# Performance work log

Hardware: AMD Instinct MI355X
Metric: run time of the kernel (lower is better)

Reference implementation:

```python
import jax, jax.numpy as jnp
import numpy as np

D_MODEL, N_LEVELS, N_HEADS, N_POINTS = 256, 3, 8, 2
HEAD_DIM = D_MODEL // N_HEADS
SPATIAL_SHAPES = np.array([[100, 100], [50, 50], [25, 25]], dtype=np.int32)
LEN_IN = int((SPATIAL_SHAPES[:, 0] * SPATIAL_SHAPES[:, 1]).sum())  # 13125
BS, NQ = 16, 900


def setup_inputs() -> dict:
    key = jax.random.key(0)
    ks = jax.random.split(key, 12)
    s = 1.0 / np.sqrt(D_MODEL)
    return {
        "query": jax.random.normal(ks[0], (BS, NQ, N_LEVELS, D_MODEL), jnp.float32),
        "reference_points": jax.random.uniform(ks[1], (BS, NQ, N_LEVELS, 2), jnp.float32),
        "input_flatten": jax.random.normal(ks[2], (BS, LEN_IN, D_MODEL), jnp.float32),
        "input_spatial_shapes": jnp.asarray(SPATIAL_SHAPES),
        "W_value": jax.random.normal(ks[3], (D_MODEL, D_MODEL), jnp.float32) * s,
        "b_value": jnp.zeros((D_MODEL,), jnp.float32),
        "W_off": jax.random.normal(ks[4], (D_MODEL, N_HEADS * N_LEVELS * N_POINTS * 2), jnp.float32) * s * 0.1,
        "b_off": jax.random.normal(ks[5], (N_HEADS * N_LEVELS * N_POINTS * 2,), jnp.float32) * 0.5,
        "W_attn": jax.random.normal(ks[6], (D_MODEL, N_HEADS * N_LEVELS * N_POINTS), jnp.float32) * s,
        "b_attn": jnp.zeros((N_HEADS * N_LEVELS * N_POINTS,), jnp.float32),
        "W_out": jax.random.normal(ks[7], (D_MODEL, D_MODEL), jnp.float32) * s,
        "b_out": jnp.zeros((D_MODEL,), jnp.float32),
    }


def _bilinear_sample(v, loc, H, W):
    """v: (bs, nh, H*W, hd); loc in [0,1]: (bs, nh, N, 2). Zero-pad out of range."""
    hd = v.shape[-1]
    x = loc[..., 0] * W - 0.5
    y = loc[..., 1] * H - 0.5
    x0 = jnp.floor(x)
    y0 = jnp.floor(y)
    out = jnp.zeros(x.shape + (hd,), v.dtype)
    for dx in (0, 1):
        for dy in (0, 1):
            xi = x0 + dx
            yi = y0 + dy
            wgt = (1.0 - jnp.abs(x - xi)) * (1.0 - jnp.abs(y - yi))
            valid = (xi >= 0) & (xi <= W - 1) & (yi >= 0) & (yi <= H - 1)
            xi_c = jnp.clip(xi, 0, W - 1).astype(jnp.int32)
            yi_c = jnp.clip(yi, 0, H - 1).astype(jnp.int32)
            idx = yi_c * W + xi_c  # (bs, nh, N)
            idx = jnp.broadcast_to(idx[..., None], idx.shape + (hd,))
            g = jnp.take_along_axis(v, idx, axis=2)  # (bs, nh, N, hd)
            out = out + g * (wgt * valid.astype(wgt.dtype))[..., None]
    return out


def reference(query, reference_points, input_flatten, input_spatial_shapes,
              W_value, b_value, W_off, b_off, W_attn, b_attn, W_out, b_out):
    bs, nq, fl, _ = query.shape
    shapes = np.asarray(input_spatial_shapes)  # static pyramid shapes

    # value projection: (bs, Len, nh, hd)
    value = (input_flatten @ W_value + b_value).reshape(bs, -1, N_HEADS, HEAD_DIM)

    # sampling offsets: (bs, nq, fl, nh, nl, np, 2)
    offsets = (query @ W_off + b_off).reshape(bs, nq, fl, N_HEADS, N_LEVELS, N_POINTS, 2)
    # attention weights softmax over (nl*np): (bs, nq, fl, nh, nl, np)
    attn = (query @ W_attn + b_attn).reshape(bs, nq, fl, N_HEADS, N_LEVELS * N_POINTS)
    attn = jax.nn.softmax(attn, axis=-1).reshape(bs, nq, fl, N_HEADS, N_LEVELS, N_POINTS)

    # normalized sampling locations: ref + offset / (W_l, H_l)
    normalizer = jnp.asarray(shapes[:, ::-1], jnp.float32)  # (nl, 2) = (W, H)
    loc = reference_points[:, :, :, None, None, None, :] + offsets / normalizer[None, None, None, None, :, None, :]

    splits = np.cumsum([h * w for h, w in shapes])[:-1]
    value_list = jnp.split(value, splits, axis=1)

    out = jnp.zeros((bs, N_HEADS, nq, fl, HEAD_DIM), value.dtype)
    for lvl, (H, W) in enumerate(shapes):
        H, W = int(H), int(W)
        v = jnp.transpose(value_list[lvl], (0, 2, 1, 3))  # (bs, nh, H*W, hd)
        loc_l = jnp.transpose(loc[:, :, :, :, lvl], (0, 3, 1, 2, 4, 5))  # (bs, nh, nq, fl, np, 2)
        loc_flat = loc_l.reshape(bs, N_HEADS, nq * fl * N_POINTS, 2)
        sampled = _bilinear_sample(v, loc_flat, H, W).reshape(bs, N_HEADS, nq, fl, N_POINTS, HEAD_DIM)
        w = jnp.transpose(attn[:, :, :, :, lvl], (0, 3, 1, 2, 4))  # (bs, nh, nq, fl, np)
        out = out + jnp.einsum("bhqfpd,bhqfp->bhqfd", sampled, w)

    out = jnp.transpose(out, (0, 2, 3, 1, 4)).reshape(bs, nq, fl, D_MODEL)
    return out @ W_out + b_out
```

## Files before the change

### kernel.cpp

```cpp
#include <hip/hip_runtime.h>
#include <math.h>

#define D_MODEL   256
#define N_HEADS   8
#define HEAD_DIM  32
#define N_LEVELS  3
#define N_POINTS  2
#define BS        16
#define NQ        900
#define LEN_IN    13125
#define M_Q       (BS * NQ * N_LEVELS)
#define M_V       (BS * LEN_IN)
#define NCAT      144
#define NCATP     256

typedef _Float16 f16x8 __attribute__((ext_vector_type(8)));
typedef _Float16 f16x4 __attribute__((ext_vector_type(4)));
typedef float f32x4 __attribute__((ext_vector_type(4)));

__global__ __launch_bounds__(256) void convert_weight_kernel(
    const float* __restrict__ W, _Float16* __restrict__ Wph,
    _Float16* __restrict__ Wpl, int N, int Npad) {
  const int idx = blockIdx.x * 256 + threadIdx.x;
  if (idx >= Npad * 256) return;
  const int n = idx >> 8;
  const int k = idx & 255;
  const float v = (n < N) ? W[(size_t)k * N + n] : 0.0f;
  const _Float16 h = (_Float16)v;
  const int dst = (((n >> 4) * 32) + (k >> 3)) * 128 + (n & 15) * 8 + (k & 7);
  Wph[dst] = h;
  Wpl[dst] = (_Float16)(v - (float)h);
}

__global__ __launch_bounds__(256) void convert_cat_kernel(
    const float* __restrict__ Woff, const float* __restrict__ Wattn,
    const float* __restrict__ boff, const float* __restrict__ battn,
    _Float16* __restrict__ Wph, _Float16* __restrict__ Wpl,
    float* __restrict__ bcat) {
  const int idx = blockIdx.x * 256 + threadIdx.x;
  if (idx >= NCATP * 256) return;
  const int n = idx >> 8;
  const int k = idx & 255;
  float v = 0.0f;
  if (n < 96) v = Woff[(size_t)k * 96 + n];
  else if (n < NCAT) v = Wattn[(size_t)k * 48 + (n - 96)];
  const _Float16 h = (_Float16)v;
  const int dst = (((n >> 4) * 32) + (k >> 3)) * 128 + (n & 15) * 8 + (k & 7);
  Wph[dst] = h;
  Wpl[dst] = (_Float16)(v - (float)h);
  if (idx < NCAT) bcat[idx] = (idx < 96) ? boff[idx] : battn[idx - 96];
}

template <int FC, int TAG>
__global__ __launch_bounds__(256, 4) void gemm4_kernel(
    const float* __restrict__ A, const _Float16* __restrict__ Bph,
    const _Float16* __restrict__ Bpl, const float* __restrict__ bias,
    float* __restrict__ C, int M, int N) {
  constexpr int K = 256;
  __shared__ _Float16 AhL[64 * 128];
  __shared__ _Float16 AlL[64 * 128];

  const int tid = threadIdx.x;
  const int wid = tid >> 6;
  const int lane = tid & 63;
  const int bx = blockIdx.x;
  const int bm = blockIdx.y * 64;
  const int rsel = lane & 15;
  const int q = (lane >> 4) & 3;
  const int swzx = (rsel & 7) << 4;

  char* AhB = (char*)AhL;
  char* AlB = (char*)AlL;

  const _Float16* bph[FC];
  const _Float16* bpl[FC];
#pragma unroll
  for (int fc = 0; fc < FC; ++fc) {
    const int g = bx * 8 + wid * 2 + fc;
    bph[fc] = Bph + (size_t)g * 4096 + lane * 8;
    bpl[fc] = Bpl + (size_t)g * 4096 + lane * 8;
  }

  f32x4 acc[4][FC];
#pragma unroll
  for (int fr = 0; fr < 4; ++fr)
#pragma unroll
    for (int fc = 0; fc < FC; ++fc) acc[fr][fc] = (f32x4)0.0f;

#pragma unroll
  for (int c = 0; c < 2; ++c) {
    if (c == 1) __syncthreads();
#pragma unroll
    for (int it = 0; it < 8; ++it) {
      const int i = it * 1024 + tid * 4;
      const int row = i >> 7;
      const int col = i & 127;
      float4 v = make_float4(0.f, 0.f, 0.f, 0.f);
      if (bm + row < M)
        v = *reinterpret_cast<const float4*>(
            &A[(size_t)(bm + row) * K + c * 128 + col]);
      f16x4 h, l;
      h[0] = (_Float16)v.x; l[0] = (_Float16)(v.x - (float)h[0]);
      h[1] = (_Float16)v.y; l[1] = (_Float16)(v.y - (float)h[1]);
      h[2] = (_Float16)v.z; l[2] = (_Float16)(v.z - (float)h[2]);
      h[3] = (_Float16)v.w; l[3] = (_Float16)(v.w - (float)h[3]);
      const int byt = row * 256 + ((col * 2) ^ ((row & 7) << 4));
      *reinterpret_cast<f16x4*>(AhB + byt) = h;
      *reinterpret_cast<f16x4*>(AlB + byt) = l;
    }
    __syncthreads();

#pragma unroll
    for (int sl = 0; sl < 4; ++sl) {
      const int s = c * 4 + sl;
      f16x8 bh[FC], bl[FC], afh[4], afl[4];
#pragma unroll
      for (int fc = 0; fc < FC; ++fc) {
        bh[fc] = *reinterpret_cast<const f16x8*>(bph[fc] + s * 512);
        bl[fc] = *reinterpret_cast<const f16x8*>(bpl[fc] + s * 512);
      }
#pragma unroll
      for (int fr = 0; fr < 4; ++fr) {
        const int row = fr * 16 + rsel;
        const int byt = row * 256 + ((sl * 64 + q * 16) ^ swzx);
        afh[fr] = *reinterpret_cast<const f16x8*>(AhB + byt);
        afl[fr] = *reinterpret_cast<const f16x8*>(AlB + byt);
      }
      __builtin_amdgcn_s_setprio(1);
#pragma unroll
      for (int fr = 0; fr < 4; ++fr)
#pragma unroll
        for (int fc = 0; fc < FC; ++fc)
          acc[fr][fc] = __builtin_amdgcn_mfma_f32_16x16x32_f16(
              afh[fr], bh[fc], acc[fr][fc], 0, 0, 0);
#pragma unroll
      for (int fr = 0; fr < 4; ++fr)
#pragma unroll
        for (int fc = 0; fc < FC; ++fc)
          acc[fr][fc] = __builtin_amdgcn_mfma_f32_16x16x32_f16(
              afh[fr], bl[fc], acc[fr][fc], 0, 0, 0);
#pragma unroll
      for (int fr = 0; fr < 4; ++fr)
#pragma unroll
        for (int fc = 0; fc < FC; ++fc)
          acc[fr][fc] = __builtin_amdgcn_mfma_f32_16x16x32_f16(
              afl[fr], bh[fc], acc[fr][fc], 0, 0, 0);
      __builtin_amdgcn_s_setprio(0);
    }
  }

  const int colbase = bx * 128 + wid * 32;
  float bs_[FC];
#pragma unroll
  for (int fc = 0; fc < FC; ++fc) {
    const int col = colbase + fc * 16 + rsel;
    bs_[fc] = (col < N) ? bias[col] : 0.0f;
  }
#pragma unroll
  for (int fr = 0; fr < 4; ++fr)
#pragma unroll
    for (int i = 0; i < 4; ++i) {
      const int row = bm + fr * 16 + (lane >> 4) * 4 + i;
      if (row >= M) continue;
#pragma unroll
      for (int fc = 0; fc < FC; ++fc) {
        const int col = colbase + fc * 16 + rsel;
        if (col < N) C[(size_t)row * N + col] = acc[fr][fc][i] + bs_[fc];
      }
    }
}

__global__ __launch_bounds__(256) void sample2_kernel(
    const float* __restrict__ value, const float* __restrict__ refpts,
    const float* __restrict__ offs_attn, float* __restrict__ out_mid) {
  __shared__ int4   s_off[144];
  __shared__ float4 s_w[144];

  const int bq = blockIdx.x;
  const int b = bq / NQ;
  const int tid = threadIdx.x;

  if (tid < 144) {
    const int fl = tid / 48;
    const int rem = tid - fl * 48;
    const int h = rem / 6;
    const int j = rem - h * 6;
    const int l = j >> 1;

    const int LVL_W[3] = {100, 50, 25};
    const int LVL_BASE[3] = {0, 10000, 12500};
    const int W = LVL_W[l];
    const int base = LVL_BASE[l];
    const float fW = (float)W, fH = (float)W;

    const int row = bq * 3 + fl;
    const float* oa = offs_attn + (size_t)row * NCAT;

    float aw[6];
    float mx = -INFINITY;
#pragma unroll
    for (int jj = 0; jj < 6; ++jj) {
      aw[jj] = oa[96 + h * 6 + jj];
      mx = fmaxf(mx, aw[jj]);
    }
    float ssum = 0.f;
#pragma unroll
    for (int jj = 0; jj < 6; ++jj) ssum += expf(aw[jj] - mx);
    const float wa = expf(aw[j] - mx) / ssum;

    const float rx = refpts[(size_t)row * 2 + 0];
    const float ry = refpts[(size_t)row * 2 + 1];
    const float ox = oa[h * 12 + j * 2 + 0];
    const float oy = oa[h * 12 + j * 2 + 1];
    const float x = (rx + ox / fW) * fW - 0.5f;
    const float y = (ry + oy / fH) * fH - 0.5f;
    const float x0 = floorf(x);
    const float y0 = floorf(y);

    int offv[4];
    float wv[4];
#pragma unroll
    for (int dy = 0; dy < 2; ++dy)
#pragma unroll
      for (int dx = 0; dx < 2; ++dx) {
        const float xi = x0 + (float)dx;
        const float yi = y0 + (float)dy;
        const float wgt = (1.0f - fabsf(x - xi)) * (1.0f - fabsf(y - yi));
        const bool valid = (xi >= 0.f) && (xi <= fW - 1.f) &&
                           (yi >= 0.f) && (yi <= fH - 1.f);
        const int xic = (int)fminf(fmaxf(xi, 0.f), fW - 1.f);
        const int yic = (int)fminf(fmaxf(yi, 0.f), fH - 1.f);
        const int pos = base + yic * W + xic;
        offv[dy * 2 + dx] = pos * 1024;
        wv[dy * 2 + dx] = valid ? wgt * wa : 0.0f;
      }
    s_off[tid] = make_int4(offv[0], offv[1], offv[2], offv[3]);
    s_w[tid] = make_float4(wv[0], wv[1], wv[2], wv[3]);
  }
  __syncthreads();

  const int h = tid >> 5;
  const int d = tid & 31;
  const char* vb = (const char*)value +
                   ((size_t)b * LEN_IN * 256 + h * 32 + d) * 4;

#pragma unroll
  for (int fl = 0; fl < 3; ++fl) {
    float acc = 0.f;
#pragma unroll
    for (int j = 0; j < 6; ++j) {
      const int rec = fl * 48 + h * 6 + j;
      const int4 o = s_off[rec];
      const float4 w = s_w[rec];
      acc = fmaf(w.x, *(const float*)(vb + o.x), acc);
      acc = fmaf(w.y, *(const float*)(vb + o.y), acc);
      acc = fmaf(w.z, *(const float*)(vb + o.z), acc);
      acc = fmaf(w.w, *(const float*)(vb + o.w), acc);
    }
    out_mid[((size_t)bq * 3 + fl) * 256 + tid] = acc;
  }
}

extern "C" void kernel_launch(void* const* d_in, const int* in_sizes, int n_in,
                              void* d_out, int out_size, void* d_ws,
                              size_t ws_size, hipStream_t stream) {
  const float* query   = (const float*)d_in[0];
  const float* refpts  = (const float*)d_in[1];
  const float* in_flat = (const float*)d_in[2];
  const float* W_value = (const float*)d_in[4];
  const float* b_value = (const float*)d_in[5];
  const float* W_off   = (const float*)d_in[6];
  const float* b_off   = (const float*)d_in[7];
  const float* W_attn  = (const float*)d_in[8];
  const float* b_attn  = (const float*)d_in[9];
  const float* W_out   = (const float*)d_in[10];
  const float* b_out   = (const float*)d_in[11];
  float* out = (float*)d_out;

  char* ws = (char*)d_ws;
  float* value     = (float*)ws; ws += (size_t)M_V * 256 * sizeof(float);
  float* out_mid   = (float*)ws; ws += (size_t)M_Q * 256 * sizeof(float);
  float* offs_attn = (float*)ws; ws += (size_t)M_Q * NCAT * sizeof(float);
  _Float16* Wvh = (_Float16*)ws; ws += 256 * 256 * sizeof(_Float16);
  _Float16* Wvl = (_Float16*)ws; ws += 256 * 256 * sizeof(_Float16);
  _Float16* Woh = (_Float16*)ws; ws += 256 * 256 * sizeof(_Float16);
  _Float16* Wol = (_Float16*)ws; ws += 256 * 256 * sizeof(_Float16);
  _Float16* Wch = (_Float16*)ws; ws += NCATP * 256 * sizeof(_Float16);
  _Float16* Wcl = (_Float16*)ws; ws += NCATP * 256 * sizeof(_Float16);
  float* bcat   = (float*)ws;    ws += 256 * sizeof(float);

  const dim3 blk(256);

  convert_weight_kernel<<<dim3(256), blk, 0, stream>>>(W_value, Wvh, Wvl, 256, 256);
  convert_weight_kernel<<<dim3(256), blk, 0, stream>>>(W_out,   Woh, Wol, 256, 256);
  convert_cat_kernel<<<dim3(NCATP), blk, 0, stream>>>(W_off, W_attn, b_off, b_attn,
                                                      Wch, Wcl, bcat);

  gemm4_kernel<2, 1><<<dim3(2, (M_V + 63) / 64), blk, 0, stream>>>(
      in_flat, Wvh, Wvl, b_value, value, M_V, 256);

  gemm4_kernel<2, 2><<<dim3(2, (M_Q + 63) / 64), blk, 0, stream>>>(
      query, Wch, Wcl, bcat, offs_attn, M_Q, NCAT);

  sample2_kernel<<<dim3(BS * NQ), blk, 0, stream>>>(value, refpts, offs_attn,
                                                    out_mid);

  gemm4_kernel<2, 3><<<dim3(2, (M_Q + 63) / 64), blk, 0, stream>>>(
      out_mid, Woh, Wol, b_out, out, M_Q, 256);
}
```

Measured before the change: 777.8 us.

## Store value projection and sampled output in fp16 to halve memory traffic

The value projection is now written as fp16 instead of fp32, and the sampling kernel reads fp16 values and writes its intermediate output as fp16. A new GEMM variant takes fp16 A directly, skipping the hi/lo split of A, and keeps only the hi/lo split of the weights. This roughly halves the bytes moved for the large value tensor and the intermediate, cutting both write and gather bandwidth. The cost is precision: activations are rounded to fp16, which may raise error against the fp32 reference.

```diff
diff --git a/kernel.cpp b/kernel.cpp
--- a/kernel.cpp
+++ b/kernel.cpp
@@ -51,11 +51,11 @@
   if (idx < NCAT) bcat[idx] = (idx < 96) ? boff[idx] : battn[idx - 96];
 }
 
-template <int FC, int TAG>
+template <int FC, int TAG, typename OutT>
 __global__ __launch_bounds__(256, 4) void gemm4_kernel(
     const float* __restrict__ A, const _Float16* __restrict__ Bph,
     const _Float16* __restrict__ Bpl, const float* __restrict__ bias,
-    float* __restrict__ C, int M, int N) {
+    OutT* __restrict__ C, int M, int N) {
   constexpr int K = 256;
   __shared__ _Float16 AhL[64 * 128];
   __shared__ _Float16 AlL[64 * 128];
@@ -165,14 +165,118 @@
 #pragma unroll
       for (int fc = 0; fc < FC; ++fc) {
         const int col = colbase + fc * 16 + rsel;
+        if (col < N) C[(size_t)row * N + col] = (OutT)(acc[fr][fc][i] + bs_[fc]);
+      }
+    }
+}
+
+template <int FC>
+__global__ __launch_bounds__(256, 4) void gemm5_kernel(
+    const _Float16* __restrict__ A, const _Float16* __restrict__ Bph,
+    const _Float16* __restrict__ Bpl, const float* __restrict__ bias,
+    float* __restrict__ C, int M, int N) {
+  constexpr int K = 256;
+  __shared__ _Float16 AhL[64 * 128];
+
+  const int tid = threadIdx.x;
+  const int wid = tid >> 6;
+  const int lane = tid & 63;
+  const int bx = blockIdx.x;
+  const int bm = blockIdx.y * 64;
+  const int rsel = lane & 15;
+  const int q = (lane >> 4) & 3;
+  const int swzx = (rsel & 7) << 4;
+
+  char* AhB = (char*)AhL;
+
+  const _Float16* bph[FC];
+  const _Float16* bpl[FC];
+#pragma unroll
+  for (int fc = 0; fc < FC; ++fc) {
+    const int g = bx * 8 + wid * 2 + fc;
+    bph[fc] = Bph + (size_t)g * 4096 + lane * 8;
+    bpl[fc] = Bpl + (size_t)g * 4096 + lane * 8;
+  }
+
+  f32x4 acc[4][FC];
+#pragma unroll
+  for (int fr = 0; fr < 4; ++fr)
+#pragma unroll
+    for (int fc = 0; fc < FC; ++fc) acc[fr][fc] = (f32x4)0.0f;
+
+#pragma unroll
+  for (int c = 0; c < 2; ++c) {
+    if (c == 1) __syncthreads();
+#pragma unroll
+    for (int it = 0; it < 4; ++it) {
+      const int i = it * 2048 + tid * 8;
+      const int row = i >> 7;
+      const int col = i & 127;
+      f16x8 v = (f16x8)(_Float16)0;
+      if (bm + row < M)
+        v = *reinterpret_cast<const f16x8*>(
+            &A[(size_t)(bm + row) * K + c * 128 + col]);
+      const int byt = row * 256 + ((col * 2) ^ ((row & 7) << 4));
+      *reinterpret_cast<f16x8*>(AhB + byt) = v;
+    }
+    __syncthreads();
+
+#pragma unroll
+    for (int sl = 0; sl < 4; ++sl) {
+      const int s = c * 4 + sl;
+      f16x8 bh[FC], bl[FC], afh[4];
+#pragma unroll
+      for (int fc = 0; fc < FC; ++fc) {
+        bh[fc] = *reinterpret_cast<const f16x8*>(bph[fc] + s * 512);
+        bl[fc] = *reinterpret_cast<const f16x8*>(bpl[fc] + s * 512);
+      }
+#pragma unroll
+      for (int fr = 0; fr < 4; ++fr) {
+        const int row = fr * 16 + rsel;
+        const int byt = row * 256 + ((sl * 64 + q * 16) ^ swzx);
+        afh[fr] = *reinterpret_cast<const f16x8*>(AhB + byt);
+      }
+      __builtin_amdgcn_s_setprio(1);
+#pragma unroll
+      for (int fr = 0; fr < 4; ++fr)
+#pragma unroll
+        for (int fc = 0; fc < FC; ++fc)
+          acc[fr][fc] = __builtin_amdgcn_mfma_f32_16x16x32_f16(
+              afh[fr], bh[fc], acc[fr][fc], 0, 0, 0);
+#pragma unroll
+      for (int fr = 0; fr < 4; ++fr)
+#pragma unroll
+        for (int fc = 0; fc < FC; ++fc)
+          acc[fr][fc] = __builtin_amdgcn_mfma_f32_16x16x32_f16(
+              afh[fr], bl[fc], acc[fr][fc], 0, 0, 0);
+      __builtin_amdgcn_s_setprio(0);
+    }
+  }
+
+  const int colbase = bx * 128 + wid * 32;
+  float bs_[FC];
+#pragma unroll
+  for (int fc = 0; fc < FC; ++fc) {
+    const int col = colbase + fc * 16 + rsel;
+    bs_[fc] = (col < N) ? bias[col] : 0.0f;
+  }
+#pragma unroll
+  for (int fr = 0; fr < 4; ++fr)
+#pragma unroll
+    for (int i = 0; i < 4; ++i) {
+      const int row = bm + fr * 16 + (lane >> 4) * 4 + i;
+      if (row >= M) continue;
+#pragma unroll
+      for (int fc = 0; fc < FC; ++fc) {
+        const int col = colbase + fc * 16 + rsel;
         if (col < N) C[(size_t)row * N + col] = acc[fr][fc][i] + bs_[fc];
       }
     }
 }
 
-__global__ __launch_bounds__(256) void sample2_kernel(
-    const float* __restrict__ value, const float* __restrict__ refpts,
-    const float* __restrict__ offs_attn, float* __restrict__ out_mid) {
+__global__ __launch_bounds__(256) void sample3_kernel(
+    const _Float16* __restrict__ value, const float* __restrict__ refpts,
+    const float* __restrict__ offs_attn, _Float16* __restrict__ out_mid) {
   __shared__ int4   s_off[144];
   __shared__ float4 s_w[144];
 
@@ -231,7 +335,7 @@
         const int xic = (int)fminf(fmaxf(xi, 0.f), fW - 1.f);
         const int yic = (int)fminf(fmaxf(yi, 0.f), fH - 1.f);
         const int pos = base + yic * W + xic;
-        offv[dy * 2 + dx] = pos * 1024;
+        offv[dy * 2 + dx] = pos * 512;
         wv[dy * 2 + dx] = valid ? wgt * wa : 0.0f;
       }
     s_off[tid] = make_int4(offv[0], offv[1], offv[2], offv[3]);
@@ -242,7 +346,7 @@
   const int h = tid >> 5;
   const int d = tid & 31;
   const char* vb = (const char*)value +
-                   ((size_t)b * LEN_IN * 256 + h * 32 + d) * 4;
+                   ((size_t)b * LEN_IN * 256 + h * 32 + d) * 2;
 
 #pragma unroll
   for (int fl = 0; fl < 3; ++fl) {
@@ -252,12 +356,12 @@
       const int rec = fl * 48 + h * 6 + j;
       const int4 o = s_off[rec];
       const float4 w = s_w[rec];
-      acc = fmaf(w.x, *(const float*)(vb + o.x), acc);
-      acc = fmaf(w.y, *(const float*)(vb + o.y), acc);
-      acc = fmaf(w.z, *(const float*)(vb + o.z), acc);
-      acc = fmaf(w.w, *(const float*)(vb + o.w), acc);
-    }
-    out_mid[((size_t)bq * 3 + fl) * 256 + tid] = acc;
+      acc = fmaf(w.x, (float)*(const _Float16*)(vb + o.x), acc);
+      acc = fmaf(w.y, (float)*(const _Float16*)(vb + o.y), acc);
+      acc = fmaf(w.z, (float)*(const _Float16*)(vb + o.z), acc);
+      acc = fmaf(w.w, (float)*(const _Float16*)(vb + o.w), acc);
+    }
+    out_mid[((size_t)bq * 3 + fl) * 256 + tid] = (_Float16)acc;
   }
 }
 
@@ -278,9 +382,9 @@
   float* out = (float*)d_out;
 
   char* ws = (char*)d_ws;
-  float* value     = (float*)ws; ws += (size_t)M_V * 256 * sizeof(float);
-  float* out_mid   = (float*)ws; ws += (size_t)M_Q * 256 * sizeof(float);
-  float* offs_attn = (float*)ws; ws += (size_t)M_Q * NCAT * sizeof(float);
+  _Float16* value_h  = (_Float16*)ws; ws += (size_t)M_V * 256 * sizeof(_Float16);
+  _Float16* out_mid  = (_Float16*)ws; ws += (size_t)M_Q * 256 * sizeof(_Float16);
+  float* offs_attn   = (float*)ws;    ws += (size_t)M_Q * NCAT * sizeof(float);
   _Float16* Wvh = (_Float16*)ws; ws += 256 * 256 * sizeof(_Float16);
   _Float16* Wvl = (_Float16*)ws; ws += 256 * 256 * sizeof(_Float16);
   _Float16* Woh = (_Float16*)ws; ws += 256 * 256 * sizeof(_Float16);
@@ -296,15 +400,15 @@
   convert_cat_kernel<<<dim3(NCATP), blk, 0, stream>>>(W_off, W_attn, b_off, b_attn,
                                                       Wch, Wcl, bcat);
 
-  gemm4_kernel<2, 1><<<dim3(2, (M_V + 63) / 64), blk, 0, stream>>>(
-      in_flat, Wvh, Wvl, b_value, value, M_V, 256);
-
-  gemm4_kernel<2, 2><<<dim3(2, (M_Q + 63) / 64), blk, 0, stream>>>(
+  gemm4_kernel<2, 1, _Float16><<<dim3(2, (M_V + 63) / 64), blk, 0, stream>>>(
+      in_flat, Wvh, Wvl, b_value, value_h, M_V, 256);
+
+  gemm4_kernel<2, 2, float><<<dim3(2, (M_Q + 63) / 64), blk, 0, stream>>>(
       query, Wch, Wcl, bcat, offs_attn, M_Q, NCAT);
 
-  sample2_kernel<<<dim3(BS * NQ), blk, 0, stream>>>(value, refpts, offs_attn,
+  sample3_kernel<<<dim3(BS * NQ), blk, 0, stream>>>(value_h, refpts, offs_attn,
                                                     out_mid);
 
-  gemm4_kernel<2, 3><<<dim3(2, (M_Q + 63) / 64), blk, 0, stream>>>(
+  gemm5_kernel<2><<<dim3(2, (M_Q + 63) / 64), blk, 0, stream>>>(
       out_mid, Woh, Wol, b_out, out, M_Q, 256);
 }
```

New measurement: 717.8 us. 1.08x faster.
